# Optimization experiments

Measured on AMD Instinct MI355X. Metric: run time of the kernel, lower is better.

Reference implementation:

```python
import jax, jax.numpy as jnp
import numpy as np

B, S, F = 2048, 1024, 64  # batch, n_support, num_features

def setup_inputs() -> dict:
    key = jax.random.key(0)
    k1, k2, k3, k4 = jax.random.split(key, 4)
    X = jax.random.normal(k1, (B, F), dtype=jnp.float32)
    support = jax.random.normal(k2, (S, F), dtype=jnp.float32)
    W = jax.random.normal(k3, (1, S), dtype=jnp.float32) * (1.0 / np.sqrt(S))
    b = jax.random.normal(k4, (1,), dtype=jnp.float32)
    return {"X": X, "support": support, "W": W, "b": b}

def reference(X, support, W, b):
    # Quantum kernel: product states from RX rotations are tensor products of
    # [cos(t/2), -i sin(t/2)] per qubit; the overlap factorizes exactly as
    # <psi(a)|psi(b)> = prod_f cos((a_f - b_f)/2), hence
    # K[i,j] = |overlap|^2 = prod_f cos^2((X[i,f] - support[j,f]) / 2).
    diff = X[:, None, :] - support[None, :, :]          # [B, S, F]
    c = jnp.cos(diff * 0.5)
    K = jnp.prod(c * c, axis=-1)                        # [B, S]
    # Linear head: K @ W^T + b, then squeeze(-1) -> [B]
    return K @ W[0] + b[0]
```

## Files before the change

kernel.cpp:

```cpp
#include <hip/hip_runtime.h>
#include <math.h>

#define B_ 2048
#define S_ 1024
#define F_ 64


__global__ __launch_bounds__(256) void qkr_prep(
    const float* __restrict__ X, const float* __restrict__ Sup,
    const float* __restrict__ b,
    float* __restrict__ CxT, float* __restrict__ SxT,
    float* __restrict__ CsT, float* __restrict__ SsT,
    float* __restrict__ out)
{
    const int blk = blockIdx.x;
    const int t = threadIdx.x;
    if (blk == 48) {
        const float bv = b[0];
        #pragma unroll
        for (int k = 0; k < 8; ++k) out[k * 256 + t] = bv;
        return;
    }
    __shared__ float sc[64][65];
    __shared__ float sn[64][65];
    const bool isX = blk < 32;
    const float* __restrict__ src = isX ? X : Sup;
    float* __restrict__ Cd = isX ? CxT : CsT;
    float* __restrict__ Sd = isX ? SxT : SsT;
    const int N = isX ? B_ : S_;
    const int r0 = (isX ? blk : blk - 32) * 64;
    const float scale = isX ? 0.5f : 1.0f;
    const int l = t & 15, g = t >> 4;

    #pragma unroll
    for (int k = 0; k < 4; ++k) {
        const int r = k * 16 + g;
        const float4 v = *(const float4*)&src[(size_t)(r0 + r) * F_ + l * 4];
        float cv, sv;
        sincosf(v.x, &sv, &cv); sc[l*4+0][r] = scale*cv; sn[l*4+0][r] = scale*sv;
        sincosf(v.y, &sv, &cv); sc[l*4+1][r] = scale*cv; sn[l*4+1][r] = scale*sv;
        sincosf(v.z, &sv, &cv); sc[l*4+2][r] = scale*cv; sn[l*4+2][r] = scale*sv;
        sincosf(v.w, &sv, &cv); sc[l*4+3][r] = scale*cv; sn[l*4+3][r] = scale*sv;
    }
    __syncthreads();
    #pragma unroll
    for (int k = 0; k < 4; ++k) {
        const int f = k * 16 + g;
        float4 c, s;
        c.x = sc[f][l*4+0]; c.y = sc[f][l*4+1]; c.z = sc[f][l*4+2]; c.w = sc[f][l*4+3];
        s.x = sn[f][l*4+0]; s.y = sn[f][l*4+1]; s.z = sn[f][l*4+2]; s.w = sn[f][l*4+3];
        *(float4*)&Cd[(size_t)f * N + r0 + l * 4] = c;
        *(float4*)&Sd[(size_t)f * N + r0 + l * 4] = s;
    }
}

__global__ __launch_bounds__(256) void qkr_main(
    const float* __restrict__ CxT, const float* __restrict__ SxT,
    const float* __restrict__ CsT, const float* __restrict__ SsT,
    const float* __restrict__ W, float* __restrict__ out)
{
    __shared__ float sCx[64 * 64];
    __shared__ float sSx[64 * 64];
    __shared__ float sCs[64 * 64];
    __shared__ float sSs[64 * 64];

    const int t = threadIdx.x;
    const int i0 = blockIdx.x * 64;
    const int j0 = blockIdx.y * 64;
    const int l = t & 15, g = t >> 4;

    #pragma unroll
    for (int k = 0; k < 4; ++k) {
        const int f = k * 16 + g;
        *(float4*)&sCx[f * 64 + l * 4] = *(const float4*)&CxT[(size_t)f * B_ + i0 + l * 4];
        *(float4*)&sSx[f * 64 + l * 4] = *(const float4*)&SxT[(size_t)f * B_ + i0 + l * 4];
        *(float4*)&sCs[f * 64 + l * 4] = *(const float4*)&CsT[(size_t)f * S_ + j0 + l * 4];
        *(float4*)&sSs[f * 64 + l * 4] = *(const float4*)&SsT[(size_t)f * S_ + j0 + l * 4];
    }
    __syncthreads();

    const int tx = l;
    const int ty = g;

    float p[4][4];
    #pragma unroll
    for (int a = 0; a < 4; ++a)
        #pragma unroll
        for (int c = 0; c < 4; ++c) p[a][c] = 1.0f;

    #pragma unroll 8
    for (int f = 0; f < 64; ++f) {
        const float4 cx4 = *(const float4*)&sCx[f * 64 + ty * 4];
        const float4 sx4 = *(const float4*)&sSx[f * 64 + ty * 4];
        const float4 cs4 = *(const float4*)&sCs[f * 64 + tx * 4];
        const float4 ss4 = *(const float4*)&sSs[f * 64 + tx * 4];
        const float cx[4] = {cx4.x, cx4.y, cx4.z, cx4.w};
        const float sx[4] = {sx4.x, sx4.y, sx4.z, sx4.w};
        const float cs[4] = {cs4.x, cs4.y, cs4.z, cs4.w};
        const float ss[4] = {ss4.x, ss4.y, ss4.z, ss4.w};
        #pragma unroll
        for (int a = 0; a < 4; ++a) {
            #pragma unroll
            for (int c = 0; c < 4; ++c) {
                float term = fmaf(cx[a], cs[c], 0.5f);
                term = fmaf(sx[a], ss[c], term);
                p[a][c] *= term;
            }
        }
    }

    const float4 w4 = *(const float4*)&W[j0 + tx * 4];
    const float wj[4] = {w4.x, w4.y, w4.z, w4.w};
    #pragma unroll
    for (int a = 0; a < 4; ++a) {
        float acc = p[a][0] * wj[0];
        acc = fmaf(p[a][1], wj[1], acc);
        acc = fmaf(p[a][2], wj[2], acc);
        acc = fmaf(p[a][3], wj[3], acc);
        acc += __shfl_xor(acc, 1);
        acc += __shfl_xor(acc, 2);
        acc += __shfl_xor(acc, 4);
        acc += __shfl_xor(acc, 8);
        if (tx == 0) atomicAdd(&out[i0 + ty * 4 + a], acc);
    }
}

extern "C" void kernel_launch(void* const* d_in, const int* in_sizes, int n_in,
                              void* d_out, int out_size, void* d_ws, size_t ws_size,
                              hipStream_t stream) {
    const float* X   = (const float*)d_in[0];
    const float* Sup = (const float*)d_in[1];
    const float* W   = (const float*)d_in[2];
    const float* b   = (const float*)d_in[3];
    float* out = (float*)d_out;

    float* ws  = (float*)d_ws;
    float* CxT = ws;
    float* SxT = ws + 131072;
    float* CsT = ws + 262144;
    float* SsT = ws + 327680;

    qkr_prep<<<dim3(49), dim3(256), 0, stream>>>(X, Sup, b, CxT, SxT, CsT, SsT, out);
    qkr_main<<<dim3(32, 16), dim3(256), 0, stream>>>(CxT, SxT, CsT, SsT, W, out);
}
```

Measured before the change: 73.16 us.

## Pack cos/sin as fp16 pairs and use fdot2 in main loop

```diff
diff --git a/kernel.cpp b/kernel.cpp
--- a/kernel.cpp
+++ b/kernel.cpp
@@ -5,64 +5,55 @@
 #define S_ 1024
 #define F_ 64
 
+typedef _Float16 half2_t __attribute__((ext_vector_type(2)));
+
 
 __global__ __launch_bounds__(256) void qkr_prep(
     const float* __restrict__ X, const float* __restrict__ Sup,
     const float* __restrict__ b,
-    float* __restrict__ CxT, float* __restrict__ SxT,
-    float* __restrict__ CsT, float* __restrict__ SsT,
+    half2_t* __restrict__ PxT, half2_t* __restrict__ PsT,
     float* __restrict__ out)
 {
     const int blk = blockIdx.x;
     const int t = threadIdx.x;
-    if (blk == 48) {
+    if (blk == 96) {
         const float bv = b[0];
         #pragma unroll
         for (int k = 0; k < 8; ++k) out[k * 256 + t] = bv;
         return;
     }
-    __shared__ float sc[64][65];
-    __shared__ float sn[64][65];
-    const bool isX = blk < 32;
+    __shared__ half2_t sh2[64][33];
+    const bool isX = blk < 64;
     const float* __restrict__ src = isX ? X : Sup;
-    float* __restrict__ Cd = isX ? CxT : CsT;
-    float* __restrict__ Sd = isX ? SxT : SsT;
+    half2_t* __restrict__ dst = isX ? PxT : PsT;
     const int N = isX ? B_ : S_;
-    const int r0 = (isX ? blk : blk - 32) * 64;
+    const int r0 = (isX ? blk : blk - 64) * 32;
     const float scale = isX ? 0.5f : 1.0f;
     const int l = t & 15, g = t >> 4;
 
     #pragma unroll
-    for (int k = 0; k < 4; ++k) {
+    for (int k = 0; k < 2; ++k) {
         const int r = k * 16 + g;
         const float4 v = *(const float4*)&src[(size_t)(r0 + r) * F_ + l * 4];
         float cv, sv;
-        sincosf(v.x, &sv, &cv); sc[l*4+0][r] = scale*cv; sn[l*4+0][r] = scale*sv;
-        sincosf(v.y, &sv, &cv); sc[l*4+1][r] = scale*cv; sn[l*4+1][r] = scale*sv;
-        sincosf(v.z, &sv, &cv); sc[l*4+2][r] = scale*cv; sn[l*4+2][r] = scale*sv;
-        sincosf(v.w, &sv, &cv); sc[l*4+3][r] = scale*cv; sn[l*4+3][r] = scale*sv;
+        __sincosf(v.x, &sv, &cv); sh2[l*4+0][r] = (half2_t){(_Float16)(scale*cv), (_Float16)(scale*sv)};
+        __sincosf(v.y, &sv, &cv); sh2[l*4+1][r] = (half2_t){(_Float16)(scale*cv), (_Float16)(scale*sv)};
+        __sincosf(v.z, &sv, &cv); sh2[l*4+2][r] = (half2_t){(_Float16)(scale*cv), (_Float16)(scale*sv)};
+        __sincosf(v.w, &sv, &cv); sh2[l*4+3][r] = (half2_t){(_Float16)(scale*cv), (_Float16)(scale*sv)};
     }
     __syncthreads();
+    const int f = t >> 2, seg = t & 3;
+    half2_t* __restrict__ drow = &dst[(size_t)f * N + r0 + seg * 8];
     #pragma unroll
-    for (int k = 0; k < 4; ++k) {
-        const int f = k * 16 + g;
-        float4 c, s;
-        c.x = sc[f][l*4+0]; c.y = sc[f][l*4+1]; c.z = sc[f][l*4+2]; c.w = sc[f][l*4+3];
-        s.x = sn[f][l*4+0]; s.y = sn[f][l*4+1]; s.z = sn[f][l*4+2]; s.w = sn[f][l*4+3];
-        *(float4*)&Cd[(size_t)f * N + r0 + l * 4] = c;
-        *(float4*)&Sd[(size_t)f * N + r0 + l * 4] = s;
-    }
+    for (int q = 0; q < 8; ++q) drow[q] = sh2[f][seg * 8 + q];
 }
 
-__global__ __launch_bounds__(256) void qkr_main(
-    const float* __restrict__ CxT, const float* __restrict__ SxT,
-    const float* __restrict__ CsT, const float* __restrict__ SsT,
+__global__ __launch_bounds__(256, 2) void qkr_main(
+    const half2_t* __restrict__ PxT, const half2_t* __restrict__ PsT,
     const float* __restrict__ W, float* __restrict__ out)
 {
-    __shared__ float sCx[64 * 64];
-    __shared__ float sSx[64 * 64];
-    __shared__ float sCs[64 * 64];
-    __shared__ float sSs[64 * 64];
+    __shared__ half2_t sX[64][64];
+    __shared__ half2_t sS[64][64];
 
     const int t = threadIdx.x;
     const int i0 = blockIdx.x * 64;
@@ -72,10 +63,8 @@
     #pragma unroll
     for (int k = 0; k < 4; ++k) {
         const int f = k * 16 + g;
-        *(float4*)&sCx[f * 64 + l * 4] = *(const float4*)&CxT[(size_t)f * B_ + i0 + l * 4];
-        *(float4*)&sSx[f * 64 + l * 4] = *(const float4*)&SxT[(size_t)f * B_ + i0 + l * 4];
-        *(float4*)&sCs[f * 64 + l * 4] = *(const float4*)&CsT[(size_t)f * S_ + j0 + l * 4];
-        *(float4*)&sSs[f * 64 + l * 4] = *(const float4*)&SsT[(size_t)f * S_ + j0 + l * 4];
+        *(float4*)&sX[f][l * 4] = *(const float4*)&PxT[(size_t)f * B_ + i0 + l * 4];
+        *(float4*)&sS[f][l * 4] = *(const float4*)&PsT[(size_t)f * S_ + j0 + l * 4];
     }
     __syncthreads();
 
@@ -88,22 +77,21 @@
         #pragma unroll
         for (int c = 0; c < 4; ++c) p[a][c] = 1.0f;
 
-    #pragma unroll 8
+    #pragma unroll 4
     for (int f = 0; f < 64; ++f) {
-        const float4 cx4 = *(const float4*)&sCx[f * 64 + ty * 4];
-        const float4 sx4 = *(const float4*)&sSx[f * 64 + ty * 4];
-        const float4 cs4 = *(const float4*)&sCs[f * 64 + tx * 4];
-        const float4 ss4 = *(const float4*)&sSs[f * 64 + tx * 4];
-        const float cx[4] = {cx4.x, cx4.y, cx4.z, cx4.w};
-        const float sx[4] = {sx4.x, sx4.y, sx4.z, sx4.w};
-        const float cs[4] = {cs4.x, cs4.y, cs4.z, cs4.w};
-        const float ss[4] = {ss4.x, ss4.y, ss4.z, ss4.w};
+        union { float4 v; half2_t h[4]; } ux, us;
+        ux.v = *(const float4*)&sX[f][ty * 4];
+        us.v = *(const float4*)&sS[f][tx * 4];
         #pragma unroll
         for (int a = 0; a < 4; ++a) {
             #pragma unroll
             for (int c = 0; c < 4; ++c) {
-                float term = fmaf(cx[a], cs[c], 0.5f);
-                term = fmaf(sx[a], ss[c], term);
+#if __has_builtin(__builtin_amdgcn_fdot2)
+                const float term = __builtin_amdgcn_fdot2(ux.h[a], us.h[c], 0.5f, false);
+#else
+                const float term = 0.5f + (float)ux.h[a].x * (float)us.h[c].x
+                                        + (float)ux.h[a].y * (float)us.h[c].y;
+#endif
                 p[a][c] *= term;
             }
         }
@@ -134,12 +122,10 @@
     const float* b   = (const float*)d_in[3];
     float* out = (float*)d_out;
 
-    float* ws  = (float*)d_ws;
-    float* CxT = ws;
-    float* SxT = ws + 131072;
-    float* CsT = ws + 262144;
-    float* SsT = ws + 327680;
+    char* ws = (char*)d_ws;
+    half2_t* PxT = (half2_t*)ws;
+    half2_t* PsT = (half2_t*)(ws + 524288);
 
-    qkr_prep<<<dim3(49), dim3(256), 0, stream>>>(X, Sup, b, CxT, SxT, CsT, SsT, out);
-    qkr_main<<<dim3(32, 16), dim3(256), 0, stream>>>(CxT, SxT, CsT, SsT, W, out);
+    qkr_prep<<<dim3(97), dim3(256), 0, stream>>>(X, Sup, b, PxT, PsT, out);
+    qkr_main<<<dim3(32, 16), dim3(256), 0, stream>>>(PxT, PsT, W, out);
 }
```

Result: faster. 71.37 us (-2.4%).
